# Kernel optimization log

Hardware: AMD Instinct MI355X
Metric: run time of the kernel (lower is better)

## Reference

```python
import jax, jax.numpy as jnp
import numpy as np

B = 8192
COND_DIM = 64
OUT_DIM = 64      # output_dim (joint velocity dim)
ACT_DIM = 8       # action_dim (latent action dim)
H1, H2 = 256, 256


def setup_inputs() -> dict:
    key = jax.random.key(0)
    ks = jax.random.split(key, 8)
    inp = {
        "cond_inp": jax.random.normal(ks[0], (B, COND_DIM), dtype=jnp.float32),
        "low_level_action": jax.random.normal(ks[1], (B, OUT_DIM), dtype=jnp.float32),
        # MLP params: cond_dim -> 256 -> 256 -> action_dim*output_dim
        "W1": jax.random.normal(ks[2], (COND_DIM, H1), dtype=jnp.float32) / np.sqrt(COND_DIM),
        "b1": jnp.zeros((H1,), dtype=jnp.float32),
        "W2": jax.random.normal(ks[3], (H1, H2), dtype=jnp.float32) / np.sqrt(H1),
        "b2": jnp.zeros((H2,), dtype=jnp.float32),
        "W3": jax.random.normal(ks[4], (H2, ACT_DIM * OUT_DIM), dtype=jnp.float32) / np.sqrt(H2),
        "b3": jnp.zeros((ACT_DIM * OUT_DIM,), dtype=jnp.float32),
    }
    return inp


def _householder(Hcols):
    # Hcols: [B, n, k]; chain of k batched Householder reflections.
    n = Hcols.shape[1]
    k = Hcols.shape[2]
    I = jnp.eye(n, dtype=Hcols.dtype)
    Q = jnp.broadcast_to(I, (Hcols.shape[0], n, n))
    for c in range(k):  # small fixed unroll over latent action columns
        v = Hcols[:, :, c]                                  # [B, n]
        vvT = jnp.einsum('bi,bj->bij', v, v)                # [B, n, n]
        vTv = jnp.einsum('bi,bi->b', v, v)[:, None, None]   # [B, 1, 1]
        Qi = I - 2.0 * vvT / vTv
        Q = jnp.matmul(Qi, Q)
    return Q[:, :, :k]


def reference(cond_inp, low_level_action, W1, b1, W2, b2, W3, b3):
    # MLP h(cond_inp)
    x = jnp.tanh(cond_inp @ W1 + b1)
    x = jnp.tanh(x @ W2 + b2)
    x = x @ W3 + b3                                    # [B, act*out]
    Hcols = x.reshape(-1, OUT_DIM, ACT_DIM)            # [B, out, act]
    scl_map = _householder(Hcols)                      # [B, out, act], orthonormal cols
    # best action: a* = S^T qdot ; reconstruction: qdot_hat = S a*
    a_star = jnp.einsum('bnk,bn->bk', scl_map, low_level_action)   # [B, act]
    q_dot_hat = jnp.einsum('bnk,bk->bn', scl_map, a_star)          # [B, out]
    return q_dot_hat[..., None]                        # [B, out, 1] (matches tf.matmul shape)
```

## Files before the change

kernel.cpp:

```cpp
#include <hip/hip_runtime.h>

typedef float f4 __attribute__((ext_vector_type(4)));
typedef float f2 __attribute__((ext_vector_type(2)));
typedef float f32x4 __attribute__((ext_vector_type(4)));
typedef _Float16 f16x8 __attribute__((ext_vector_type(8)));

#define HSWZ16(o) ((o) ^ (((o) >> 3) & 0x70))

__global__ void prep_frags_all(const float* __restrict__ W1,
                               const float* __restrict__ W2,
                               const float* __restrict__ W3,
                               _Float16* __restrict__ dst) {
    int p = blockIdx.x;
    int q = threadIdx.x & 3, l = (threadIdx.x >> 2) & 63;
    const float* W; int K, N, lp; size_t off;
    if (p < 32)       { W = W1; K = 64;  N = 256; lp = p;       off = 0; }
    else if (p < 160) { W = W2; K = 256; N = 256; lp = p - 32;  off = 16384; }
    else              { W = W3; K = 256; N = 512; lp = p - 160; off = 81920; }
    int KT = K >> 5;
    int kt = lp % KT, nt = lp / KT;
    int k = kt * 32 + ((l >> 4) << 3) + 2 * q;
    int n = nt * 16 + (l & 15);
    size_t base = off + (size_t)lp * 512 + l * 8 + 2 * q;
    dst[base]     = (_Float16)W[k * N + n];
    dst[base + 1] = (_Float16)W[(k + 1) * N + n];
}

__device__ __forceinline__ float ftanh(float x) {
    float e = __expf(2.0f * x);
    return 1.0f - 2.0f / (e + 1.0f);
}
__device__ __forceinline__ float red32(float x) {
    x += __shfl_xor(x, 1); x += __shfl_xor(x, 2);  x += __shfl_xor(x, 4);
    x += __shfl_xor(x, 8); x += __shfl_xor(x, 16);
    return x;
}

__global__ __launch_bounds__(512, 4) void scl_mfma(
    const float* __restrict__ cond, const float* __restrict__ act,
    const float* __restrict__ b1, const float* __restrict__ b2,
    const float* __restrict__ b3,
    const _Float16* __restrict__ wf,
    float* __restrict__ out)
{
    __shared__ char smem[33792];
    _Float16* x1h = (_Float16*)smem;
    _Float16* x1l = (_Float16*)(smem + 8448);
    _Float16* x2h = (_Float16*)(smem + 16896);
    _Float16* x2l = (_Float16*)(smem + 25344);

    const int tid = threadIdx.x;
    const int w   = tid >> 6;
    const int l   = tid & 63;
    const int lr  = l & 15;
    const int lg  = l >> 4;
    const int rb  = blockIdx.x * 16;

    const f16x8* wp = (const f16x8*)wf;

    {
        f16x8 ah[2], al[2];
        #pragma unroll
        for (int kt = 0; kt < 2; ++kt) {
            const float* src = cond + (rb + lr) * 64 + kt * 32 + lg * 8;
            f4 v0 = *(const f4*)src;
            f4 v1 = *(const f4*)(src + 4);
            float vv[8] = {v0[0], v0[1], v0[2], v0[3], v1[0], v1[1], v1[2], v1[3]};
            #pragma unroll
            for (int j = 0; j < 8; ++j) {
                _Float16 hx = (_Float16)vv[j];
                ah[kt][j] = hx;
                al[kt][j] = (_Float16)(vv[j] - (float)hx);
            }
        }
        f32x4 acc[2] = {};
        #pragma unroll
        for (int ntL = 0; ntL < 2; ++ntL) {
            #pragma unroll
            for (int kt = 0; kt < 2; ++kt) {
                int pi = (w * 2 + ntL) * 2 + kt;
                f16x8 bh = wp[pi * 64 + l];
                acc[ntL] = __builtin_amdgcn_mfma_f32_16x16x32_f16(ah[kt], bh, acc[ntL], 0, 0, 0);
                acc[ntL] = __builtin_amdgcn_mfma_f32_16x16x32_f16(al[kt], bh, acc[ntL], 0, 0, 0);
            }
        }
        #pragma unroll
        for (int ntL = 0; ntL < 2; ++ntL) {
            int col = (w * 2 + ntL) * 16 + lr;
            float bb = b1[col];
            #pragma unroll
            for (int r = 0; r < 4; ++r) {
                float v = ftanh(acc[ntL][r] + bb);
                int row = lg * 4 + r;
                _Float16 hx = (_Float16)v;
                x1h[row * 264 + col] = hx;
                x1l[row * 264 + col] = (_Float16)(v - (float)hx);
            }
        }
    }
    __syncthreads();

    {
        f32x4 acc[2] = {};
        #pragma unroll 2
        for (int kt = 0; kt < 8; ++kt) {
            int cb = kt * 32 + lg * 8;
            f16x8 ah = *(const f16x8*)&x1h[lr * 264 + cb];
            f16x8 al = *(const f16x8*)&x1l[lr * 264 + cb];
            #pragma unroll
            for (int ntL = 0; ntL < 2; ++ntL) {
                int pi = (w * 2 + ntL) * 8 + kt;
                f16x8 bh = wp[2048 + pi * 64 + l];
                acc[ntL] = __builtin_amdgcn_mfma_f32_16x16x32_f16(ah, bh, acc[ntL], 0, 0, 0);
                acc[ntL] = __builtin_amdgcn_mfma_f32_16x16x32_f16(al, bh, acc[ntL], 0, 0, 0);
            }
        }
        #pragma unroll
        for (int ntL = 0; ntL < 2; ++ntL) {
            int col = (w * 2 + ntL) * 16 + lr;
            float bb = b2[col];
            #pragma unroll
            for (int r = 0; r < 4; ++r) {
                float v = ftanh(acc[ntL][r] + bb);
                int row = lg * 4 + r;
                _Float16 hx = (_Float16)v;
                x2h[row * 264 + col] = hx;
                x2l[row * 264 + col] = (_Float16)(v - (float)hx);
            }
        }
    }
    __syncthreads();

    {
        f32x4 acc[4] = {};
        #pragma unroll 2
        for (int kt = 0; kt < 8; ++kt) {
            int cb = kt * 32 + lg * 8;
            f16x8 ah = *(const f16x8*)&x2h[lr * 264 + cb];
            f16x8 al = *(const f16x8*)&x2l[lr * 264 + cb];
            #pragma unroll
            for (int ntL = 0; ntL < 4; ++ntL) {
                int pi = (w * 4 + ntL) * 8 + kt;
                f16x8 bh = wp[10240 + pi * 64 + l];
                acc[ntL] = __builtin_amdgcn_mfma_f32_16x16x32_f16(ah, bh, acc[ntL], 0, 0, 0);
                acc[ntL] = __builtin_amdgcn_mfma_f32_16x16x32_f16(al, bh, acc[ntL], 0, 0, 0);
            }
        }
        #pragma unroll
        for (int ntL = 0; ntL < 4; ++ntL) {
            int col = (w * 4 + ntL) * 16 + lr;
            float bb = b3[col];
            #pragma unroll
            for (int r = 0; r < 4; ++r) {
                int row = lg * 4 + r;
                *(_Float16*)(smem + row * 1048 + HSWZ16(col * 2)) = (_Float16)(acc[ntL][r] + bb);
            }
        }
    }
    __syncthreads();

    {
        const int c  = l & 31;
        const int rh = l >> 5;
        const int hrow = w * 2 + rh;
        const int grow = rb + hrow;
        f16x8 hv[2];
        #pragma unroll
        for (int j = 0; j < 2; ++j)
            hv[j] = *(const f16x8*)(smem + hrow * 1048 + HSWZ16(c * 32 + j * 16));
        float h[8][2];
        #pragma unroll
        for (int cc = 0; cc < 8; ++cc) {
            h[cc][0] = (float)hv[0][cc];
            h[cc][1] = (float)hv[1][cc];
        }
        float inv[8];
        #pragma unroll
        for (int cc = 0; cc < 8; ++cc) {
            float s = h[cc][0] * h[cc][0] + h[cc][1] * h[cc][1];
            inv[cc] = 2.0f / red32(s);
        }
        f2 av = *(const f2*)&act[grow * 64 + 2 * c];
        float u[2] = {av[0], av[1]};
        #pragma unroll
        for (int cc = 7; cc >= 0; --cc) {
            float d = red32(h[cc][0] * u[0] + h[cc][1] * u[1]);
            float t = inv[cc] * d;
            u[0] -= t * h[cc][0];
            u[1] -= t * h[cc][1];
        }
        float wv[2];
        wv[0] = (c < 4) ? u[0] : 0.0f;
        wv[1] = (c < 4) ? u[1] : 0.0f;
        #pragma unroll
        for (int cc = 0; cc < 8; ++cc) {
            float d = red32(h[cc][0] * wv[0] + h[cc][1] * wv[1]);
            float t = inv[cc] * d;
            wv[0] -= t * h[cc][0];
            wv[1] -= t * h[cc][1];
        }
        f2 o = {wv[0], wv[1]};
        *(f2*)&out[grow * 64 + 2 * c] = o;
    }
}

extern "C" void kernel_launch(void* const* d_in, const int* in_sizes, int n_in,
                              void* d_out, int out_size, void* d_ws, size_t ws_size,
                              hipStream_t stream) {
    const float* cond = (const float*)d_in[0];
    const float* act  = (const float*)d_in[1];
    const float* W1   = (const float*)d_in[2];
    const float* b1   = (const float*)d_in[3];
    const float* W2   = (const float*)d_in[4];
    const float* b2   = (const float*)d_in[5];
    const float* W3   = (const float*)d_in[6];
    const float* b3   = (const float*)d_in[7];
    float* outp = (float*)d_out;

    _Float16* wf = (_Float16*)d_ws;
    prep_frags_all<<<dim3(416), dim3(256), 0, stream>>>(W1, W2, W3, wf);
    scl_mfma<<<dim3(512), dim3(512), 0, stream>>>(cond, act, b1, b2, b3, wf, outp);
}
```

Baseline: 28.34 us.

## Prefetch weights and inputs into registers early, coalesce weight prep via LDS

New measurement: 26.61 us. 6.1% less time.

```diff
diff --git a/kernel.cpp b/kernel.cpp
--- a/kernel.cpp
+++ b/kernel.cpp
@@ -7,23 +7,36 @@
 
 #define HSWZ16(o) ((o) ^ (((o) >> 3) & 0x70))
 
-__global__ void prep_frags_all(const float* __restrict__ W1,
-                               const float* __restrict__ W2,
-                               const float* __restrict__ W3,
-                               _Float16* __restrict__ dst) {
-    int p = blockIdx.x;
-    int q = threadIdx.x & 3, l = (threadIdx.x >> 2) & 63;
-    const float* W; int K, N, lp; size_t off;
-    if (p < 32)       { W = W1; K = 64;  N = 256; lp = p;       off = 0; }
-    else if (p < 160) { W = W2; K = 256; N = 256; lp = p - 32;  off = 16384; }
-    else              { W = W3; K = 256; N = 512; lp = p - 160; off = 81920; }
-    int KT = K >> 5;
-    int kt = lp % KT, nt = lp / KT;
-    int k = kt * 32 + ((l >> 4) << 3) + 2 * q;
-    int n = nt * 16 + (l & 15);
-    size_t base = off + (size_t)lp * 512 + l * 8 + 2 * q;
-    dst[base]     = (_Float16)W[k * N + n];
-    dst[base + 1] = (_Float16)W[(k + 1) * N + n];
+#define BARLG() asm volatile("s_waitcnt lgkmcnt(0)\n\ts_barrier" ::: "memory")
+
+__global__ __launch_bounds__(256) void prep_frags_all(
+    const float* __restrict__ W1, const float* __restrict__ W2,
+    const float* __restrict__ W3, _Float16* __restrict__ dst) {
+    __shared__ float s[32 * 264];
+    const int b = blockIdx.x, tid = threadIdx.x;
+    const float* W; int N, kt, nh, KT; size_t off;
+    if (b < 2)       { W = W1; N = 256; KT = 2; kt = b;            nh = 0;          off = 0; }
+    else if (b < 10) { W = W2; N = 256; KT = 8; kt = b - 2;        nh = 0;          off = 16384; }
+    else             { W = W3; N = 512; KT = 8; kt = (b - 10) >> 1; nh = (b - 10) & 1; off = 81920; }
+    #pragma unroll
+    for (int rep = 0; rep < 8; ++rep) {
+        int fi = rep * 256 + tid;
+        int row = fi >> 6, c4 = fi & 63;
+        f4 v = *(const f4*)&W[(kt * 32 + row) * N + nh * 256 + c4 * 4];
+        *(f4*)&s[row * 264 + c4 * 4] = v;
+    }
+    __syncthreads();
+    const int wv = tid >> 6, l = tid & 63, lr = l & 15, lg = l >> 4;
+    #pragma unroll
+    for (int p = 0; p < 4; ++p) {
+        int lnt = wv * 4 + p;
+        f16x8 o;
+        #pragma unroll
+        for (int j = 0; j < 8; ++j)
+            o[j] = (_Float16)s[(lg * 8 + j) * 264 + lnt * 16 + lr];
+        int page = (nh * 16 + lnt) * KT + kt;
+        *(f16x8*)&dst[off + (size_t)page * 512 + l * 8] = o;
+    }
 }
 
 __device__ __forceinline__ float ftanh(float x) {
@@ -55,42 +68,61 @@
     const int lr  = l & 15;
     const int lg  = l >> 4;
     const int rb  = blockIdx.x * 16;
-
     const f16x8* wp = (const f16x8*)wf;
 
-    {
+    const int hrow = w * 2 + (l >> 5), hc = l & 31;
+    f2 av = *(const f2*)&act[(rb + hrow) * 64 + 2 * hc];
+    const float* crow = cond + (rb + lr) * 64 + lg * 8;
+    f4 c0a = *(const f4*)crow;
+    f4 c0b = *(const f4*)(crow + 4);
+    f4 c1a = *(const f4*)(crow + 32);
+    f4 c1b = *(const f4*)(crow + 36);
+    f16x8 w1f[2][2];
+    #pragma unroll
+    for (int n = 0; n < 2; ++n)
+        #pragma unroll
+        for (int kt = 0; kt < 2; ++kt)
+            w1f[n][kt] = wp[((w * 2 + n) * 2 + kt) * 64 + l];
+    f16x8 w2f[2][8];
+    #pragma unroll
+    for (int n = 0; n < 2; ++n)
+        #pragma unroll
+        for (int kt = 0; kt < 8; ++kt)
+            w2f[n][kt] = wp[2048 + ((w * 2 + n) * 8 + kt) * 64 + l];
+    float b1v[2], b2v[2], b3v[4];
+    #pragma unroll
+    for (int n = 0; n < 2; ++n) {
+        b1v[n] = b1[(w * 2 + n) * 16 + lr];
+        b2v[n] = b2[(w * 2 + n) * 16 + lr];
+    }
+    #pragma unroll
+    for (int n = 0; n < 4; ++n) b3v[n] = b3[(w * 4 + n) * 16 + lr];
+
+    {
+        float v0[8] = {c0a[0], c0a[1], c0a[2], c0a[3], c0b[0], c0b[1], c0b[2], c0b[3]};
+        float v1[8] = {c1a[0], c1a[1], c1a[2], c1a[3], c1b[0], c1b[1], c1b[2], c1b[3]};
         f16x8 ah[2], al[2];
         #pragma unroll
-        for (int kt = 0; kt < 2; ++kt) {
-            const float* src = cond + (rb + lr) * 64 + kt * 32 + lg * 8;
-            f4 v0 = *(const f4*)src;
-            f4 v1 = *(const f4*)(src + 4);
-            float vv[8] = {v0[0], v0[1], v0[2], v0[3], v1[0], v1[1], v1[2], v1[3]};
-            #pragma unroll
-            for (int j = 0; j < 8; ++j) {
-                _Float16 hx = (_Float16)vv[j];
-                ah[kt][j] = hx;
-                al[kt][j] = (_Float16)(vv[j] - (float)hx);
-            }
+        for (int j = 0; j < 8; ++j) {
+            _Float16 h0 = (_Float16)v0[j];
+            ah[0][j] = h0; al[0][j] = (_Float16)(v0[j] - (float)h0);
+            _Float16 h1 = (_Float16)v1[j];
+            ah[1][j] = h1; al[1][j] = (_Float16)(v1[j] - (float)h1);
         }
         f32x4 acc[2] = {};
         #pragma unroll
-        for (int ntL = 0; ntL < 2; ++ntL) {
+        for (int n = 0; n < 2; ++n)
             #pragma unroll
             for (int kt = 0; kt < 2; ++kt) {
-                int pi = (w * 2 + ntL) * 2 + kt;
-                f16x8 bh = wp[pi * 64 + l];
-                acc[ntL] = __builtin_amdgcn_mfma_f32_16x16x32_f16(ah[kt], bh, acc[ntL], 0, 0, 0);
-                acc[ntL] = __builtin_amdgcn_mfma_f32_16x16x32_f16(al[kt], bh, acc[ntL], 0, 0, 0);
-            }
-        }
-        #pragma unroll
-        for (int ntL = 0; ntL < 2; ++ntL) {
-            int col = (w * 2 + ntL) * 16 + lr;
-            float bb = b1[col];
+                acc[n] = __builtin_amdgcn_mfma_f32_16x16x32_f16(ah[kt], w1f[n][kt], acc[n], 0, 0, 0);
+                acc[n] = __builtin_amdgcn_mfma_f32_16x16x32_f16(al[kt], w1f[n][kt], acc[n], 0, 0, 0);
+            }
+        #pragma unroll
+        for (int n = 0; n < 2; ++n) {
+            int col = (w * 2 + n) * 16 + lr;
             #pragma unroll
             for (int r = 0; r < 4; ++r) {
-                float v = ftanh(acc[ntL][r] + bb);
+                float v = ftanh(acc[n][r] + b1v[n]);
                 int row = lg * 4 + r;
                 _Float16 hx = (_Float16)v;
                 x1h[row * 264 + col] = hx;
@@ -98,30 +130,33 @@
             }
         }
     }
-    __syncthreads();
-
+    BARLG();
+
+    f16x8 w3f[4][8];
+    #pragma unroll
+    for (int n = 0; n < 4; ++n)
+        #pragma unroll
+        for (int kt = 0; kt < 4; ++kt)
+            w3f[n][kt] = wp[10240 + ((w * 4 + n) * 8 + kt) * 64 + l];
     {
         f32x4 acc[2] = {};
-        #pragma unroll 2
+        #pragma unroll
         for (int kt = 0; kt < 8; ++kt) {
             int cb = kt * 32 + lg * 8;
             f16x8 ah = *(const f16x8*)&x1h[lr * 264 + cb];
             f16x8 al = *(const f16x8*)&x1l[lr * 264 + cb];
             #pragma unroll
-            for (int ntL = 0; ntL < 2; ++ntL) {
-                int pi = (w * 2 + ntL) * 8 + kt;
-                f16x8 bh = wp[2048 + pi * 64 + l];
-                acc[ntL] = __builtin_amdgcn_mfma_f32_16x16x32_f16(ah, bh, acc[ntL], 0, 0, 0);
-                acc[ntL] = __builtin_amdgcn_mfma_f32_16x16x32_f16(al, bh, acc[ntL], 0, 0, 0);
-            }
-        }
-        #pragma unroll
-        for (int ntL = 0; ntL < 2; ++ntL) {
-            int col = (w * 2 + ntL) * 16 + lr;
-            float bb = b2[col];
+            for (int n = 0; n < 2; ++n) {
+                acc[n] = __builtin_amdgcn_mfma_f32_16x16x32_f16(ah, w2f[n][kt], acc[n], 0, 0, 0);
+                acc[n] = __builtin_amdgcn_mfma_f32_16x16x32_f16(al, w2f[n][kt], acc[n], 0, 0, 0);
+            }
+        }
+        #pragma unroll
+        for (int n = 0; n < 2; ++n) {
+            int col = (w * 2 + n) * 16 + lr;
             #pragma unroll
             for (int r = 0; r < 4; ++r) {
-                float v = ftanh(acc[ntL][r] + bb);
+                float v = ftanh(acc[n][r] + b2v[n]);
                 int row = lg * 4 + r;
                 _Float16 hx = (_Float16)v;
                 x2h[row * 264 + col] = hx;
@@ -129,45 +164,43 @@
             }
         }
     }
-    __syncthreads();
-
+    BARLG();
+
+    #pragma unroll
+    for (int n = 0; n < 4; ++n)
+        #pragma unroll
+        for (int kt = 4; kt < 8; ++kt)
+            w3f[n][kt] = wp[10240 + ((w * 4 + n) * 8 + kt) * 64 + l];
     {
         f32x4 acc[4] = {};
-        #pragma unroll 2
+        #pragma unroll
         for (int kt = 0; kt < 8; ++kt) {
             int cb = kt * 32 + lg * 8;
             f16x8 ah = *(const f16x8*)&x2h[lr * 264 + cb];
             f16x8 al = *(const f16x8*)&x2l[lr * 264 + cb];
             #pragma unroll
-            for (int ntL = 0; ntL < 4; ++ntL) {
-                int pi = (w * 4 + ntL) * 8 + kt;
-                f16x8 bh = wp[10240 + pi * 64 + l];
-                acc[ntL] = __builtin_amdgcn_mfma_f32_16x16x32_f16(ah, bh, acc[ntL], 0, 0, 0);
-                acc[ntL] = __builtin_amdgcn_mfma_f32_16x16x32_f16(al, bh, acc[ntL], 0, 0, 0);
-            }
-        }
-        #pragma unroll
-        for (int ntL = 0; ntL < 4; ++ntL) {
-            int col = (w * 4 + ntL) * 16 + lr;
-            float bb = b3[col];
+            for (int n = 0; n < 4; ++n) {
+                acc[n] = __builtin_amdgcn_mfma_f32_16x16x32_f16(ah, w3f[n][kt], acc[n], 0, 0, 0);
+                acc[n] = __builtin_amdgcn_mfma_f32_16x16x32_f16(al, w3f[n][kt], acc[n], 0, 0, 0);
+            }
+        }
+        #pragma unroll
+        for (int n = 0; n < 4; ++n) {
+            int col = (w * 4 + n) * 16 + lr;
             #pragma unroll
             for (int r = 0; r < 4; ++r) {
                 int row = lg * 4 + r;
-                *(_Float16*)(smem + row * 1048 + HSWZ16(col * 2)) = (_Float16)(acc[ntL][r] + bb);
-            }
-        }
-    }
-    __syncthreads();
-
-    {
-        const int c  = l & 31;
-        const int rh = l >> 5;
-        const int hrow = w * 2 + rh;
-        const int grow = rb + hrow;
+                *(_Float16*)(smem + row * 1056 + HSWZ16(col * 2)) = (_Float16)(acc[n][r] + b3v[n]);
+            }
+        }
+    }
+    BARLG();
+
+    {
         f16x8 hv[2];
         #pragma unroll
         for (int j = 0; j < 2; ++j)
-            hv[j] = *(const f16x8*)(smem + hrow * 1048 + HSWZ16(c * 32 + j * 16));
+            hv[j] = *(const f16x8*)(smem + hrow * 1056 + HSWZ16(hc * 32 + j * 16));
         float h[8][2];
         #pragma unroll
         for (int cc = 0; cc < 8; ++cc) {
@@ -180,7 +213,6 @@
             float s = h[cc][0] * h[cc][0] + h[cc][1] * h[cc][1];
             inv[cc] = 2.0f / red32(s);
         }
-        f2 av = *(const f2*)&act[grow * 64 + 2 * c];
         float u[2] = {av[0], av[1]};
         #pragma unroll
         for (int cc = 7; cc >= 0; --cc) {
@@ -190,8 +222,8 @@
             u[1] -= t * h[cc][1];
         }
         float wv[2];
-        wv[0] = (c < 4) ? u[0] : 0.0f;
-        wv[1] = (c < 4) ? u[1] : 0.0f;
+        wv[0] = (hc < 4) ? u[0] : 0.0f;
+        wv[1] = (hc < 4) ? u[1] : 0.0f;
         #pragma unroll
         for (int cc = 0; cc < 8; ++cc) {
             float d = red32(h[cc][0] * wv[0] + h[cc][1] * wv[1]);
@@ -200,7 +232,7 @@
             wv[1] -= t * h[cc][1];
         }
         f2 o = {wv[0], wv[1]};
-        *(f2*)&out[grow * 64 + 2 * c] = o;
+        *(f2*)&out[(rb + hrow) * 64 + 2 * hc] = o;
     }
 }
 
@@ -218,6 +250,6 @@
     float* outp = (float*)d_out;
 
     _Float16* wf = (_Float16*)d_ws;
-    prep_frags_all<<<dim3(416), dim3(256), 0, stream>>>(W1, W2, W3, wf);
+    prep_frags_all<<<dim3(26), dim3(256), 0, stream>>>(W1, W2, W3, wf);
     scl_mfma<<<dim3(512), dim3(512), 0, stream>>>(cond, act, b1, b2, b3, wf, outp);
 }
```

## Drop hi/lo fp16 split, swizzle LDS activations, raise occupancy

Applied to the files above, without the earlier changes.

Result: slower. 29.80 us (+5.2%).

```diff
diff --git a/kernel.cpp b/kernel.cpp
--- a/kernel.cpp
+++ b/kernel.cpp
@@ -5,12 +5,16 @@
 typedef float f32x4 __attribute__((ext_vector_type(4)));
 typedef _Float16 f16x8 __attribute__((ext_vector_type(8)));
 
+__device__ __forceinline__ int XA(int row, int col) {
+    return row * 528 + ((((col >> 3) ^ (row & 7)) << 4) + ((col & 7) << 1));
+}
 #define HSWZ16(o) ((o) ^ (((o) >> 3) & 0x70))
 
-__global__ void prep_frags_all(const float* __restrict__ W1,
-                               const float* __restrict__ W2,
-                               const float* __restrict__ W3,
-                               _Float16* __restrict__ dst) {
+#define BARLG() asm volatile("s_waitcnt lgkmcnt(0)\n\ts_barrier" ::: "memory")
+
+__global__ __launch_bounds__(256) void prep_frags_all(
+    const float* __restrict__ W1, const float* __restrict__ W2,
+    const float* __restrict__ W3, _Float16* __restrict__ dst) {
     int p = blockIdx.x;
     int q = threadIdx.x & 3, l = (threadIdx.x >> 2) & 63;
     const float* W; int K, N, lp; size_t off;
@@ -36,18 +40,14 @@
     return x;
 }
 
-__global__ __launch_bounds__(512, 4) void scl_mfma(
+__global__ __launch_bounds__(512, 8) void scl_mfma(
     const float* __restrict__ cond, const float* __restrict__ act,
     const float* __restrict__ b1, const float* __restrict__ b2,
     const float* __restrict__ b3,
     const _Float16* __restrict__ wf,
     float* __restrict__ out)
 {
-    __shared__ char smem[33792];
-    _Float16* x1h = (_Float16*)smem;
-    _Float16* x1l = (_Float16*)(smem + 8448);
-    _Float16* x2h = (_Float16*)(smem + 16896);
-    _Float16* x2l = (_Float16*)(smem + 25344);
+    __shared__ char smem[16896];
 
     const int tid = threadIdx.x;
     const int w   = tid >> 6;
@@ -55,119 +55,99 @@
     const int lr  = l & 15;
     const int lg  = l >> 4;
     const int rb  = blockIdx.x * 16;
-
     const f16x8* wp = (const f16x8*)wf;
 
-    {
-        f16x8 ah[2], al[2];
+    const int hrow = w * 2 + (l >> 5), hc = l & 31;
+    f2 av = *(const f2*)&act[(rb + hrow) * 64 + 2 * hc];
+    f16x8 a1[2];
+    {
+        const float* crow = cond + (rb + lr) * 64 + lg * 8;
         #pragma unroll
         for (int kt = 0; kt < 2; ++kt) {
-            const float* src = cond + (rb + lr) * 64 + kt * 32 + lg * 8;
-            f4 v0 = *(const f4*)src;
-            f4 v1 = *(const f4*)(src + 4);
-            float vv[8] = {v0[0], v0[1], v0[2], v0[3], v1[0], v1[1], v1[2], v1[3]};
-            #pragma unroll
-            for (int j = 0; j < 8; ++j) {
-                _Float16 hx = (_Float16)vv[j];
-                ah[kt][j] = hx;
-                al[kt][j] = (_Float16)(vv[j] - (float)hx);
+            f4 va = *(const f4*)(crow + kt * 32);
+            f4 vb = *(const f4*)(crow + kt * 32 + 4);
+            #pragma unroll
+            for (int j = 0; j < 4; ++j) {
+                a1[kt][j]     = (_Float16)va[j];
+                a1[kt][4 + j] = (_Float16)vb[j];
             }
         }
-        f32x4 acc[2] = {};
-        #pragma unroll
-        for (int ntL = 0; ntL < 2; ++ntL) {
-            #pragma unroll
-            for (int kt = 0; kt < 2; ++kt) {
-                int pi = (w * 2 + ntL) * 2 + kt;
-                f16x8 bh = wp[pi * 64 + l];
-                acc[ntL] = __builtin_amdgcn_mfma_f32_16x16x32_f16(ah[kt], bh, acc[ntL], 0, 0, 0);
-                acc[ntL] = __builtin_amdgcn_mfma_f32_16x16x32_f16(al[kt], bh, acc[ntL], 0, 0, 0);
-            }
-        }
-        #pragma unroll
-        for (int ntL = 0; ntL < 2; ++ntL) {
-            int col = (w * 2 + ntL) * 16 + lr;
-            float bb = b1[col];
-            #pragma unroll
-            for (int r = 0; r < 4; ++r) {
-                float v = ftanh(acc[ntL][r] + bb);
-                int row = lg * 4 + r;
-                _Float16 hx = (_Float16)v;
-                x1h[row * 264 + col] = hx;
-                x1l[row * 264 + col] = (_Float16)(v - (float)hx);
-            }
-        }
-    }
-    __syncthreads();
-
-    {
-        f32x4 acc[2] = {};
+    }
+    float b1v[2], b2v[2], b3v[4];
+    #pragma unroll
+    for (int n = 0; n < 2; ++n) {
+        b1v[n] = b1[(2 * w + n) * 16 + lr];
+        b2v[n] = b2[(2 * w + n) * 16 + lr];
+    }
+    #pragma unroll
+    for (int n = 0; n < 4; ++n) b3v[n] = b3[(4 * w + n) * 16 + lr];
+
+    #pragma unroll
+    for (int n = 0; n < 2; ++n) {
+        f32x4 acc = {b1v[n], b1v[n], b1v[n], b1v[n]};
+        #pragma unroll
+        for (int kt = 0; kt < 2; ++kt)
+            acc = __builtin_amdgcn_mfma_f32_16x16x32_f16(
+                a1[kt], wp[((2 * w + n) * 2 + kt) * 64 + l], acc, 0, 0, 0);
+        #pragma unroll
+        for (int r = 0; r < 4; ++r) {
+            float v = ftanh(acc[r]);
+            *(_Float16*)(smem + XA(lg * 4 + r, (2 * w + n) * 16 + lr)) = (_Float16)v;
+        }
+    }
+    BARLG();
+
+    {
+        f32x4 acc[2] = {{b2v[0], b2v[0], b2v[0], b2v[0]},
+                        {b2v[1], b2v[1], b2v[1], b2v[1]}};
         #pragma unroll 2
         for (int kt = 0; kt < 8; ++kt) {
-            int cb = kt * 32 + lg * 8;
-            f16x8 ah = *(const f16x8*)&x1h[lr * 264 + cb];
-            f16x8 al = *(const f16x8*)&x1l[lr * 264 + cb];
-            #pragma unroll
-            for (int ntL = 0; ntL < 2; ++ntL) {
-                int pi = (w * 2 + ntL) * 8 + kt;
-                f16x8 bh = wp[2048 + pi * 64 + l];
-                acc[ntL] = __builtin_amdgcn_mfma_f32_16x16x32_f16(ah, bh, acc[ntL], 0, 0, 0);
-                acc[ntL] = __builtin_amdgcn_mfma_f32_16x16x32_f16(al, bh, acc[ntL], 0, 0, 0);
+            f16x8 A = *(const f16x8*)(smem + XA(lr, kt * 32 + lg * 8));
+            #pragma unroll
+            for (int n = 0; n < 2; ++n)
+                acc[n] = __builtin_amdgcn_mfma_f32_16x16x32_f16(
+                    A, wp[2048 + ((2 * w + n) * 8 + kt) * 64 + l], acc[n], 0, 0, 0);
+        }
+        #pragma unroll
+        for (int n = 0; n < 2; ++n)
+            #pragma unroll
+            for (int r = 0; r < 4; ++r) {
+                float v = ftanh(acc[n][r]);
+                *(_Float16*)(smem + 8448 + XA(lg * 4 + r, (2 * w + n) * 16 + lr)) = (_Float16)v;
             }
-        }
-        #pragma unroll
-        for (int ntL = 0; ntL < 2; ++ntL) {
-            int col = (w * 2 + ntL) * 16 + lr;
-            float bb = b2[col];
-            #pragma unroll
-            for (int r = 0; r < 4; ++r) {
-                float v = ftanh(acc[ntL][r] + bb);
-                int row = lg * 4 + r;
-                _Float16 hx = (_Float16)v;
-                x2h[row * 264 + col] = hx;
-                x2l[row * 264 + col] = (_Float16)(v - (float)hx);
-            }
-        }
-    }
-    __syncthreads();
-
-    {
-        f32x4 acc[4] = {};
-        #pragma unroll 2
+    }
+    BARLG();
+
+    {
+        f32x4 acc[4] = {{b3v[0], b3v[0], b3v[0], b3v[0]},
+                        {b3v[1], b3v[1], b3v[1], b3v[1]},
+                        {b3v[2], b3v[2], b3v[2], b3v[2]},
+                        {b3v[3], b3v[3], b3v[3], b3v[3]}};
+        #pragma unroll 1
         for (int kt = 0; kt < 8; ++kt) {
-            int cb = kt * 32 + lg * 8;
-            f16x8 ah = *(const f16x8*)&x2h[lr * 264 + cb];
-            f16x8 al = *(const f16x8*)&x2l[lr * 264 + cb];
-            #pragma unroll
-            for (int ntL = 0; ntL < 4; ++ntL) {
-                int pi = (w * 4 + ntL) * 8 + kt;
-                f16x8 bh = wp[10240 + pi * 64 + l];
-                acc[ntL] = __builtin_amdgcn_mfma_f32_16x16x32_f16(ah, bh, acc[ntL], 0, 0, 0);
-                acc[ntL] = __builtin_amdgcn_mfma_f32_16x16x32_f16(al, bh, acc[ntL], 0, 0, 0);
-            }
-        }
-        #pragma unroll
-        for (int ntL = 0; ntL < 4; ++ntL) {
-            int col = (w * 4 + ntL) * 16 + lr;
-            float bb = b3[col];
-            #pragma unroll
-            for (int r = 0; r < 4; ++r) {
-                int row = lg * 4 + r;
-                *(_Float16*)(smem + row * 1048 + HSWZ16(col * 2)) = (_Float16)(acc[ntL][r] + bb);
-            }
-        }
-    }
-    __syncthreads();
-
-    {
-        const int c  = l & 31;
-        const int rh = l >> 5;
-        const int hrow = w * 2 + rh;
-        const int grow = rb + hrow;
+            f16x8 A = *(const f16x8*)(smem + 8448 + XA(lr, kt * 32 + lg * 8));
+            #pragma unroll
+            for (int n = 0; n < 4; ++n)
+                acc[n] = __builtin_amdgcn_mfma_f32_16x16x32_f16(
+                    A, wp[10240 + ((4 * w + n) * 8 + kt) * 64 + l], acc[n], 0, 0, 0);
+        }
+        BARLG();
+        #pragma unroll
+        for (int n = 0; n < 4; ++n) {
+            int col = (4 * w + n) * 16 + lr;
+            #pragma unroll
+            for (int r = 0; r < 4; ++r)
+                *(_Float16*)(smem + (lg * 4 + r) * 1056 + HSWZ16(col * 2)) =
+                    (_Float16)acc[n][r];
+        }
+    }
+    BARLG();
+
+    {
         f16x8 hv[2];
         #pragma unroll
         for (int j = 0; j < 2; ++j)
-            hv[j] = *(const f16x8*)(smem + hrow * 1048 + HSWZ16(c * 32 + j * 16));
+            hv[j] = *(const f16x8*)(smem + hrow * 1056 + HSWZ16((2 * hc + j) * 16));
         float h[8][2];
         #pragma unroll
         for (int cc = 0; cc < 8; ++cc) {
@@ -180,7 +160,6 @@
             float s = h[cc][0] * h[cc][0] + h[cc][1] * h[cc][1];
             inv[cc] = 2.0f / red32(s);
         }
-        f2 av = *(const f2*)&act[grow * 64 + 2 * c];
         float u[2] = {av[0], av[1]};
         #pragma unroll
         for (int cc = 7; cc >= 0; --cc) {
@@ -190,8 +169,8 @@
             u[1] -= t * h[cc][1];
         }
         float wv[2];
-        wv[0] = (c < 4) ? u[0] : 0.0f;
-        wv[1] = (c < 4) ? u[1] : 0.0f;
+        wv[0] = (hc < 4) ? u[0] : 0.0f;
+        wv[1] = (hc < 4) ? u[1] : 0.0f;
         #pragma unroll
         for (int cc = 0; cc < 8; ++cc) {
             float d = red32(h[cc][0] * wv[0] + h[cc][1] * wv[1]);
@@ -200,7 +179,7 @@
             wv[1] -= t * h[cc][1];
         }
         f2 o = {wv[0], wv[1]};
-        *(f2*)&out[grow * 64 + 2 * c] = o;
+        *(f2*)&out[(rb + hrow) * 64 + 2 * hc] = o;
     }
 }
 
```
